# Kernel optimization log

Hardware: AMD Instinct MI355X
Metric: run time of the kernel (lower is better)

The kernel has to match this reference:

```python
import jax, jax.numpy as jnp
import numpy as np

INDIM = 1024
OUTDIM = 2048
BATCH = 8192


def _kaiming_uniform(key, shape):
    # torch kaiming_uniform_ default: a=sqrt(5) -> gain=sqrt(2/(1+5))=sqrt(1/3),
    # fan_in = shape[0] (first dim for 2D), bound = gain*sqrt(3/fan_in) = 1/sqrt(fan_in)
    fan_in = shape[0]
    bound = 1.0 / np.sqrt(fan_in)
    return jax.random.uniform(key, shape, dtype=jnp.float32, minval=-bound, maxval=bound)


def setup_inputs() -> dict:
    key = jax.random.key(0)
    kx, kp = jax.random.split(key)
    x = jax.random.normal(kx, (BATCH, INDIM), dtype=jnp.float32)
    prototypes = _kaiming_uniform(kp, (INDIM, OUTDIM))
    return {"x": x, "prototypes": prototypes}


def reference(x, prototypes):
    # score[b, o] = -sum_i (x[b,i] - P[i,o])^2
    #             = -(||x_b||^2 - 2 x_b . P_:,o + ||P_:,o||^2)
    x_sq = jnp.sum(x * x, axis=1, keepdims=True)          # [B, 1]
    p_sq = jnp.sum(prototypes * prototypes, axis=0)       # [O]
    cross = jnp.matmul(x, prototypes)                      # [B, O] GEMM
    return 2.0 * cross - x_sq - p_sq[None, :]
```

## Files before the change

kernel.cpp:

```cpp
#include <hip/hip_runtime.h>
#include <hip/hip_bf16.h>
#include <cstdint>

#define BATCH  8192
#define INDIM  1024
#define OUTDIM 2048

typedef float  f32x4   __attribute__((ext_vector_type(4)));
typedef float  f32x16  __attribute__((ext_vector_type(16)));
typedef __bf16 bf16x8  __attribute__((ext_vector_type(8)));
typedef unsigned short u16x4 __attribute__((ext_vector_type(4)));
typedef unsigned short u16x8 __attribute__((ext_vector_type(8)));

__device__ __forceinline__ uint16_t f2b(float f) {
    __hip_bfloat16 h = __float2bfloat16(f);
    return __builtin_bit_cast(uint16_t, h);
}

__device__ __forceinline__ void async_copy16(const void* g, void* l) {
    __builtin_amdgcn_global_load_lds(
        (__attribute__((address_space(1))) void*)(g),
        (__attribute__((address_space(3))) void*)(l),
        16, 0, 0);
}

__global__ __launch_bounds__(256) void prep_all(const float* __restrict__ x,
                                                const float* __restrict__ P,
                                                uint16_t* __restrict__ xbf,
                                                uint16_t* __restrict__ ptbf,
                                                float* __restrict__ xsq,
                                                float* __restrict__ psq) {
    const int bid = blockIdx.x;
    if (bid < 64) {
        __shared__ float tile[64][33];
        __shared__ float psums[32];
        const int tid = threadIdx.x;
        const int o0  = bid * 32;
        const int kk = tid >> 3;
        const int oq = tid & 7;
        const int so  = tid >> 3;
        const int skc = (tid & 7) * 8;
        float a4[4] = {0.f, 0.f, 0.f, 0.f};
        if (tid < 32) psums[tid] = 0.f;
        for (int k0 = 0; k0 < INDIM; k0 += 64) {
            __syncthreads();
#pragma unroll
            for (int r = 0; r < 2; ++r) {
                const int k = r * 32 + kk;
                const float4 v = *(const float4*)(P + (size_t)(k0 + k) * OUTDIM + o0 + oq * 4);
                tile[k][oq * 4 + 0] = v.x;
                tile[k][oq * 4 + 1] = v.y;
                tile[k][oq * 4 + 2] = v.z;
                tile[k][oq * 4 + 3] = v.w;
                a4[0] += v.x * v.x; a4[1] += v.y * v.y;
                a4[2] += v.z * v.z; a4[3] += v.w * v.w;
            }
            __syncthreads();
            u16x8 w;
#pragma unroll
            for (int j = 0; j < 8; ++j) w[j] = f2b(tile[skc + j][so]);
            *(u16x8*)(ptbf + (size_t)(o0 + so) * INDIM + k0 + skc) = w;
        }
#pragma unroll
        for (int e = 0; e < 4; ++e) atomicAdd(&psums[oq * 4 + e], a4[e]);
        __syncthreads();
        if (tid < 32) psq[o0 + tid] = psums[tid];
    } else {
        const int wave = threadIdx.x >> 6;
        const int lane = threadIdx.x & 63;
        const int row  = (bid - 64) * 4 + wave;
        const f32x4* src = (const f32x4*)(x + (size_t)row * INDIM);
        u16x4* dst = (u16x4*)(xbf + (size_t)row * INDIM);
        float s = 0.f;
#pragma unroll
        for (int w = 0; w < 4; ++w) {
            const f32x4 v = src[lane + w * 64];
            s += v.x * v.x + v.y * v.y + v.z * v.z + v.w * v.w;
            u16x4 o;
            o.x = f2b(v.x); o.y = f2b(v.y); o.z = f2b(v.z); o.w = f2b(v.w);
            dst[lane + w * 64] = o;
        }
#pragma unroll
        for (int off = 32; off > 0; off >>= 1) s += __shfl_down(s, off);
        if (lane == 0) xsq[row] = s;
    }
}

#define TM 128
#define TN 128
#define BK 64

__global__ __launch_bounds__(256) void gemm_ep(const uint16_t* __restrict__ xbf,
                                               const uint16_t* __restrict__ ptbf,
                                               const float* __restrict__ xsq,
                                               const float* __restrict__ psq,
                                               float* __restrict__ out) {
    __shared__ __align__(16) uint16_t As[TM * BK];
    __shared__ __align__(16) uint16_t Bs[TN * BK];

    const int tid  = threadIdx.x;
    const int m0   = blockIdx.x * TM;
    const int n0   = blockIdx.y * TN;
    const int wave = tid >> 6;
    const int lane = tid & 63;
    const int wm   = (wave >> 1) * 64;
    const int wn   = (wave & 1) * 64;
    const int l31  = lane & 31;
    const int half = lane >> 5;
    const int sw   = l31 & 7;

    f32x16 acc[2][2];
#pragma unroll
    for (int i = 0; i < 2; ++i)
#pragma unroll
        for (int j = 0; j < 2; ++j)
#pragma unroll
            for (int e = 0; e < 16; ++e) acc[i][j][e] = 0.f;

    for (int kb = 0; kb < INDIM; kb += BK) {
#pragma unroll
        for (int t = 0; t < 4; ++t) {
            const int id = t * 256 + tid;
            const int r  = id >> 3;
            const int cs = id & 7;
            const int cg = cs ^ (r & 7);
            async_copy16(xbf  + (size_t)(m0 + r) * INDIM + kb + cg * 8, As + id * 8);
            async_copy16(ptbf + (size_t)(n0 + r) * INDIM + kb + cg * 8, Bs + id * 8);
        }
        __syncthreads();

#pragma unroll
        for (int ks = 0; ks < 4; ++ks) {
            const int c = ks * 2 + half;
            bf16x8 a[2], b[2];
#pragma unroll
            for (int i = 0; i < 2; ++i)
                a[i] = *(const bf16x8*)(As + (wm + i * 32 + l31) * BK + (c ^ sw) * 8);
#pragma unroll
            for (int j = 0; j < 2; ++j)
                b[j] = *(const bf16x8*)(Bs + (wn + j * 32 + l31) * BK + (c ^ sw) * 8);
#pragma unroll
            for (int i = 0; i < 2; ++i)
#pragma unroll
                for (int j = 0; j < 2; ++j)
                    acc[i][j] = __builtin_amdgcn_mfma_f32_32x32x16_bf16(a[i], b[j], acc[i][j], 0, 0, 0);
        }
        __syncthreads();
    }

    const float* xsq_w = xsq + m0 + wm;
    const float* psq_w = psq + n0 + wn;
    float ps[2];
#pragma unroll
    for (int j = 0; j < 2; ++j) ps[j] = psq_w[j * 32 + l31];
#pragma unroll
    for (int i = 0; i < 2; ++i) {
#pragma unroll
        for (int rg = 0; rg < 16; ++rg) {
            const int rloc = (rg & 3) + 8 * (rg >> 2) + 4 * half;
            const float xs = xsq_w[i * 32 + rloc];
            float* orow = out + (size_t)(m0 + wm + i * 32 + rloc) * OUTDIM + n0 + wn + l31;
#pragma unroll
            for (int j = 0; j < 2; ++j)
                orow[j * 32] = 2.f * acc[i][j][rg] - xs - ps[j];
        }
    }
}

__global__ void fallback_kernel(const float* __restrict__ x,
                                const float* __restrict__ P,
                                float* __restrict__ out) {
    const int o = blockIdx.x * blockDim.x + threadIdx.x;
    const int b = blockIdx.y;
    float cr = 0.f, xq = 0.f, pq = 0.f;
    for (int i = 0; i < INDIM; ++i) {
        const float xv = x[(size_t)b * INDIM + i];
        const float pv = P[(size_t)i * OUTDIM + o];
        cr += xv * pv; xq += xv * xv; pq += pv * pv;
    }
    out[(size_t)b * OUTDIM + o] = 2.f * cr - xq - pq;
}

extern "C" void kernel_launch(void* const* d_in, const int* in_sizes, int n_in,
                              void* d_out, int out_size, void* d_ws, size_t ws_size,
                              hipStream_t stream) {
    (void)in_sizes; (void)n_in; (void)out_size;
    const float* x = (const float*)d_in[0];
    const float* P = (const float*)d_in[1];
    float* out = (float*)d_out;

    const size_t xbf_bytes = (size_t)BATCH * INDIM * 2;
    const size_t pt_bytes  = (size_t)OUTDIM * INDIM * 2;
    const size_t xsq_bytes = (size_t)BATCH * 4;
    const size_t psq_bytes = (size_t)OUTDIM * 4;
    const size_t need = xbf_bytes + pt_bytes + xsq_bytes + psq_bytes;

    if (ws_size < need) {
        fallback_kernel<<<dim3(OUTDIM / 256, BATCH), 256, 0, stream>>>(x, P, out);
        return;
    }

    uint16_t* xbf  = (uint16_t*)d_ws;
    uint16_t* ptbf = (uint16_t*)((char*)d_ws + xbf_bytes);
    float*    xsq  = (float*)((char*)d_ws + xbf_bytes + pt_bytes);
    float*    psq  = xsq + BATCH;

    prep_all<<<64 + BATCH / 4, 256, 0, stream>>>(x, P, xbf, ptbf, xsq, psq);
    gemm_ep<<<dim3(BATCH / TM, OUTDIM / TN), 256, 0, stream>>>(xbf, ptbf, xsq, psq, out);
}
```

Measured before the change: 140.9 us.

## Fuse x bf16 conversion and row norms into GEMM, split P prep along K

The separate x-to-bf16 prep pass and its workspace are removed. The GEMM now loads fp32 x directly, computes each row's squared norm, converts to bf16 and writes swizzled LDS itself. The P prep kernel is split across four K chunks for more parallelism, and the GEMM sums the four partial norms. This saves a full write and reread of x in bf16 (about 16MB), but each of the 16 column blocks rereads fp32 x, doubling A-side global traffic, and the A loads are now synchronous instead of async-to-LDS. The swizzle key and launch bounds also change.

```diff
diff --git a/kernel.cpp b/kernel.cpp
--- a/kernel.cpp
+++ b/kernel.cpp
@@ -9,7 +9,6 @@
 typedef float  f32x4   __attribute__((ext_vector_type(4)));
 typedef float  f32x16  __attribute__((ext_vector_type(16)));
 typedef __bf16 bf16x8  __attribute__((ext_vector_type(8)));
-typedef unsigned short u16x4 __attribute__((ext_vector_type(4)));
 typedef unsigned short u16x8 __attribute__((ext_vector_type(8)));
 
 __device__ __forceinline__ uint16_t f2b(float f) {
@@ -24,79 +23,58 @@
         16, 0, 0);
 }
 
-__global__ __launch_bounds__(256) void prep_all(const float* __restrict__ x,
-                                                const float* __restrict__ P,
-                                                uint16_t* __restrict__ xbf,
-                                                uint16_t* __restrict__ ptbf,
-                                                float* __restrict__ xsq,
-                                                float* __restrict__ psq) {
-    const int bid = blockIdx.x;
-    if (bid < 64) {
-        __shared__ float tile[64][33];
-        __shared__ float psums[32];
-        const int tid = threadIdx.x;
-        const int o0  = bid * 32;
-        const int kk = tid >> 3;
-        const int oq = tid & 7;
-        const int so  = tid >> 3;
-        const int skc = (tid & 7) * 8;
-        float a4[4] = {0.f, 0.f, 0.f, 0.f};
-        if (tid < 32) psums[tid] = 0.f;
-        for (int k0 = 0; k0 < INDIM; k0 += 64) {
-            __syncthreads();
-#pragma unroll
-            for (int r = 0; r < 2; ++r) {
-                const int k = r * 32 + kk;
-                const float4 v = *(const float4*)(P + (size_t)(k0 + k) * OUTDIM + o0 + oq * 4);
-                tile[k][oq * 4 + 0] = v.x;
-                tile[k][oq * 4 + 1] = v.y;
-                tile[k][oq * 4 + 2] = v.z;
-                tile[k][oq * 4 + 3] = v.w;
-                a4[0] += v.x * v.x; a4[1] += v.y * v.y;
-                a4[2] += v.z * v.z; a4[3] += v.w * v.w;
-            }
-            __syncthreads();
-            u16x8 w;
-#pragma unroll
-            for (int j = 0; j < 8; ++j) w[j] = f2b(tile[skc + j][so]);
-            *(u16x8*)(ptbf + (size_t)(o0 + so) * INDIM + k0 + skc) = w;
-        }
-#pragma unroll
-        for (int e = 0; e < 4; ++e) atomicAdd(&psums[oq * 4 + e], a4[e]);
-        __syncthreads();
-        if (tid < 32) psq[o0 + tid] = psums[tid];
-    } else {
-        const int wave = threadIdx.x >> 6;
-        const int lane = threadIdx.x & 63;
-        const int row  = (bid - 64) * 4 + wave;
-        const f32x4* src = (const f32x4*)(x + (size_t)row * INDIM);
-        u16x4* dst = (u16x4*)(xbf + (size_t)row * INDIM);
-        float s = 0.f;
-#pragma unroll
-        for (int w = 0; w < 4; ++w) {
-            const f32x4 v = src[lane + w * 64];
-            s += v.x * v.x + v.y * v.y + v.z * v.z + v.w * v.w;
-            u16x4 o;
-            o.x = f2b(v.x); o.y = f2b(v.y); o.z = f2b(v.z); o.w = f2b(v.w);
-            dst[lane + w * 64] = o;
-        }
-#pragma unroll
-        for (int off = 32; off > 0; off >>= 1) s += __shfl_down(s, off);
-        if (lane == 0) xsq[row] = s;
-    }
+__device__ __forceinline__ int swkey(int r) { return (r ^ (r >> 3)) & 7; }
+
+__global__ __launch_bounds__(256) void prep_p(const float* __restrict__ P,
+                                              uint16_t* __restrict__ ptbf,
+                                              float* __restrict__ psq_part) {
+    __shared__ float tile[64][33];
+    __shared__ float psums[32];
+    const int tid = threadIdx.x;
+    const int o0  = blockIdx.x * 32;
+    const int k0  = blockIdx.y * 256;
+    const int kk  = tid >> 3;
+    const int oq  = tid & 7;
+    const int so  = tid >> 3;
+    const int skc = (tid & 7) * 8;
+    float a4[4] = {0.f, 0.f, 0.f, 0.f};
+    if (tid < 32) psums[tid] = 0.f;
+    for (int st = 0; st < 4; ++st) {
+        __syncthreads();
+#pragma unroll
+        for (int r2 = 0; r2 < 2; ++r2) {
+            const int k = r2 * 32 + kk;
+            const float4 v = *(const float4*)(P + (size_t)(k0 + st * 64 + k) * OUTDIM + o0 + oq * 4);
+            tile[k][oq * 4 + 0] = v.x;
+            tile[k][oq * 4 + 1] = v.y;
+            tile[k][oq * 4 + 2] = v.z;
+            tile[k][oq * 4 + 3] = v.w;
+            a4[0] += v.x * v.x; a4[1] += v.y * v.y;
+            a4[2] += v.z * v.z; a4[3] += v.w * v.w;
+        }
+        __syncthreads();
+        u16x8 w;
+#pragma unroll
+        for (int j = 0; j < 8; ++j) w[j] = f2b(tile[skc + j][so]);
+        *(u16x8*)(ptbf + (size_t)(o0 + so) * INDIM + k0 + st * 64 + skc) = w;
+    }
+#pragma unroll
+    for (int e = 0; e < 4; ++e) atomicAdd(&psums[oq * 4 + e], a4[e]);
+    __syncthreads();
+    if (tid < 32) psq_part[(size_t)blockIdx.y * OUTDIM + o0 + tid] = psums[tid];
 }
 
 #define TM 128
 #define TN 128
 #define BK 64
 
-__global__ __launch_bounds__(256) void gemm_ep(const uint16_t* __restrict__ xbf,
-                                               const uint16_t* __restrict__ ptbf,
-                                               const float* __restrict__ xsq,
-                                               const float* __restrict__ psq,
-                                               float* __restrict__ out) {
+__global__ __launch_bounds__(256, 3) void gemm_ep(const float* __restrict__ x,
+                                                  const uint16_t* __restrict__ ptbf,
+                                                  const float* __restrict__ psq_part,
+                                                  float* __restrict__ out) {
     __shared__ __align__(16) uint16_t As[TM * BK];
     __shared__ __align__(16) uint16_t Bs[TN * BK];
+    __shared__ float xs_tile[TM];
 
     const int tid  = threadIdx.x;
     const int m0   = blockIdx.x * TM;
@@ -107,7 +85,13 @@
     const int wn   = (wave & 1) * 64;
     const int l31  = lane & 31;
     const int half = lane >> 5;
-    const int sw   = l31 & 7;
+
+    const int ar = tid >> 1;
+    const int ah = tid & 1;
+    const int akey = swkey(ar);
+    const float* xrow = x + (size_t)(m0 + ar) * INDIM + ah * 32;
+    uint16_t* As_row = As + ar * BK;
+    float xs_acc = 0.f;
 
     f32x16 acc[2][2];
 #pragma unroll
@@ -123,9 +107,28 @@
             const int id = t * 256 + tid;
             const int r  = id >> 3;
             const int cs = id & 7;
-            const int cg = cs ^ (r & 7);
-            async_copy16(xbf  + (size_t)(m0 + r) * INDIM + kb + cg * 8, As + id * 8);
+            const int cg = cs ^ swkey(r);
             async_copy16(ptbf + (size_t)(n0 + r) * INDIM + kb + cg * 8, Bs + id * 8);
+        }
+        const float4* src = (const float4*)(xrow + kb);
+#pragma unroll
+        for (int p = 0; p < 2; ++p) {
+            float4 f0 = src[p * 4 + 0];
+            float4 f1 = src[p * 4 + 1];
+            float4 f2 = src[p * 4 + 2];
+            float4 f3 = src[p * 4 + 3];
+            xs_acc += f0.x * f0.x + f0.y * f0.y + f0.z * f0.z + f0.w * f0.w
+                    + f1.x * f1.x + f1.y * f1.y + f1.z * f1.z + f1.w * f1.w
+                    + f2.x * f2.x + f2.y * f2.y + f2.z * f2.z + f2.w * f2.w
+                    + f3.x * f3.x + f3.y * f3.y + f3.z * f3.z + f3.w * f3.w;
+            u16x8 w0, w1;
+            w0[0] = f2b(f0.x); w0[1] = f2b(f0.y); w0[2] = f2b(f0.z); w0[3] = f2b(f0.w);
+            w0[4] = f2b(f1.x); w0[5] = f2b(f1.y); w0[6] = f2b(f1.z); w0[7] = f2b(f1.w);
+            w1[0] = f2b(f2.x); w1[1] = f2b(f2.y); w1[2] = f2b(f2.z); w1[3] = f2b(f2.w);
+            w1[4] = f2b(f3.x); w1[5] = f2b(f3.y); w1[6] = f2b(f3.z); w1[7] = f2b(f3.w);
+            const int c0 = ah * 4 + p * 2;
+            *(u16x8*)(As_row + ((c0 ^ akey) * 8))       = w0;
+            *(u16x8*)(As_row + (((c0 + 1) ^ akey) * 8)) = w1;
         }
         __syncthreads();
 
@@ -134,11 +137,15 @@
             const int c = ks * 2 + half;
             bf16x8 a[2], b[2];
 #pragma unroll
-            for (int i = 0; i < 2; ++i)
-                a[i] = *(const bf16x8*)(As + (wm + i * 32 + l31) * BK + (c ^ sw) * 8);
-#pragma unroll
-            for (int j = 0; j < 2; ++j)
-                b[j] = *(const bf16x8*)(Bs + (wn + j * 32 + l31) * BK + (c ^ sw) * 8);
+            for (int i = 0; i < 2; ++i) {
+                const int r = wm + i * 32 + l31;
+                a[i] = *(const bf16x8*)(As + r * BK + (c ^ swkey(r)) * 8);
+            }
+#pragma unroll
+            for (int j = 0; j < 2; ++j) {
+                const int r = wn + j * 32 + l31;
+                b[j] = *(const bf16x8*)(Bs + r * BK + (c ^ swkey(r)) * 8);
+            }
 #pragma unroll
             for (int i = 0; i < 2; ++i)
 #pragma unroll
@@ -148,17 +155,23 @@
         __syncthreads();
     }
 
-    const float* xsq_w = xsq + m0 + wm;
-    const float* psq_w = psq + n0 + wn;
+    const float xs2 = xs_acc + __shfl_down(xs_acc, 1);
+    if (ah == 0) xs_tile[ar] = xs2;
+    __syncthreads();
+
     float ps[2];
 #pragma unroll
-    for (int j = 0; j < 2; ++j) ps[j] = psq_w[j * 32 + l31];
+    for (int j = 0; j < 2; ++j) {
+        const int n = n0 + wn + j * 32 + l31;
+        ps[j] = psq_part[n] + psq_part[OUTDIM + n] +
+                psq_part[2 * OUTDIM + n] + psq_part[3 * OUTDIM + n];
+    }
 #pragma unroll
     for (int i = 0; i < 2; ++i) {
 #pragma unroll
         for (int rg = 0; rg < 16; ++rg) {
             const int rloc = (rg & 3) + 8 * (rg >> 2) + 4 * half;
-            const float xs = xsq_w[i * 32 + rloc];
+            const float xs = xs_tile[wm + i * 32 + rloc];
             float* orow = out + (size_t)(m0 + wm + i * 32 + rloc) * OUTDIM + n0 + wn + l31;
 #pragma unroll
             for (int j = 0; j < 2; ++j)
@@ -189,22 +202,18 @@
     const float* P = (const float*)d_in[1];
     float* out = (float*)d_out;
 
-    const size_t xbf_bytes = (size_t)BATCH * INDIM * 2;
     const size_t pt_bytes  = (size_t)OUTDIM * INDIM * 2;
-    const size_t xsq_bytes = (size_t)BATCH * 4;
-    const size_t psq_bytes = (size_t)OUTDIM * 4;
-    const size_t need = xbf_bytes + pt_bytes + xsq_bytes + psq_bytes;
+    const size_t psq_bytes = (size_t)4 * OUTDIM * 4;
+    const size_t need = pt_bytes + psq_bytes;
 
     if (ws_size < need) {
         fallback_kernel<<<dim3(OUTDIM / 256, BATCH), 256, 0, stream>>>(x, P, out);
         return;
     }
 
-    uint16_t* xbf  = (uint16_t*)d_ws;
-    uint16_t* ptbf = (uint16_t*)((char*)d_ws + xbf_bytes);
-    float*    xsq  = (float*)((char*)d_ws + xbf_bytes + pt_bytes);
-    float*    psq  = xsq + BATCH;
-
-    prep_all<<<64 + BATCH / 4, 256, 0, stream>>>(x, P, xbf, ptbf, xsq, psq);
-    gemm_ep<<<dim3(BATCH / TM, OUTDIM / TN), 256, 0, stream>>>(xbf, ptbf, xsq, psq, out);
-}
+    uint16_t* ptbf     = (uint16_t*)d_ws;
+    float*    psq_part = (float*)((char*)d_ws + pt_bytes);
+
+    prep_p<<<dim3(OUTDIM / 32, INDIM / 256), 256, 0, stream>>>(P, ptbf, psq_part);
+    gemm_ep<<<dim3(BATCH / TM, OUTDIM / TN), 256, 0, stream>>>(x, ptbf, psq_part, out);
+}
```

Measured after the change: 186.3 us. +32.3%, slower.
